# Kernel optimization log

Measured on AMD Instinct MI355X. Metric: run time of the kernel, lower is better.

## Reference

```python
import jax, jax.numpy as jnp
import numpy as np

B, T, D, H = 2, 2048, 1024, 4
DK, DV = 1024, 2048          # key_dim = d_model*expand_k, value_dim = d_model*expand_v
HK, HV = DK // H, DV // H    # 256, 512 per-head dims
LR = 16                      # gate_low_rank_dim
EPS = 1e-5
GATE_NORM = 16.0             # gate_logit_normalizer


def _xavier(k, shape, gain):
    fan_in, fan_out = shape
    lim = gain * np.sqrt(6.0 / (fan_in + fan_out))
    return jax.random.uniform(k, shape, jnp.float32, -lim, lim)


def setup_inputs() -> dict:
    key = jax.random.key(0)
    ks = jax.random.split(key, 10)
    g_qkv = 2 ** (-2.5)
    return {
        "x": jax.random.normal(ks[0], (B, T, D), jnp.float32),
        "Wq": _xavier(ks[1], (D, DK), g_qkv),
        "Wk": _xavier(ks[2], (D, DK), g_qkv),
        "Wv": _xavier(ks[3], (D, DV), g_qkv),
        "Wg": _xavier(ks[4], (D, DV), g_qkv),
        "gk_w1": _xavier(ks[5], (D, LR), g_qkv),
        "gk_w2": _xavier(ks[6], (LR, DK), g_qkv),
        "gk_b": jnp.zeros((DK,), jnp.float32),
        "Wo": _xavier(ks[7], (DV, D), 2 ** (-1)),
        "rms_w": jnp.ones((HV,), jnp.float32),
    }


def _gla_scan(q, k, v, g):
    # q,k,g: [T, hk]; v: [T, hv]. Recurrence S_t = diag(exp(g_t)) S_{t-1} + k_t v_t^T; o_t = q_t @ S_t
    S0 = jnp.zeros((q.shape[-1], v.shape[-1]), q.dtype)

    def step(S, inp):
        qt, kt, vt, gt = inp
        S = jnp.exp(gt)[:, None] * S + kt[:, None] * vt[None, :]
        return S, qt @ S

    return jax.lax.scan(step, S0, (q, k, v, g))[1]  # [T, hv]


def _forward(x, Wq, Wk, Wv, Wg, gk_w1, gk_w2, gk_b, Wo, rms_w):
    b, t = x.shape[0], x.shape[1]
    scale = HK ** -0.5
    # projections -> [b, h, t, d_head]
    q = (x @ Wq).reshape(b, t, H, HK).transpose(0, 2, 1, 3) * scale
    k = (x @ Wk).reshape(b, t, H, HK).transpose(0, 2, 1, 3)
    v = (x @ Wv).reshape(b, t, H, HV).transpose(0, 2, 1, 3)
    # low-rank forget gate, log-space, fp32
    gl = (x @ gk_w1) @ gk_w2 + gk_b
    g = (jax.nn.log_sigmoid(gl.astype(jnp.float32)) / GATE_NORM)
    g = g.reshape(b, t, H, HK).transpose(0, 2, 1, 3)
    # per-(batch, head) linear-attention recurrence
    o = jax.vmap(jax.vmap(_gla_scan))(q, k, v, g)  # [b, h, t, hv]
    # group RMSNorm over head_v_dim
    o = o.transpose(0, 2, 1, 3)  # [b, t, h, hv]
    o = o * jax.lax.rsqrt(jnp.mean(o * o, axis=-1, keepdims=True) + EPS) * rms_w
    # output gate (swish) + out projection
    o = o.reshape(b, t, DV) * jax.nn.silu(x @ Wg)
    return o @ Wo  # [b, t, d_model]


def reference(x, Wq, Wk, Wv, Wg, gk_w1, gk_w2, gk_b, Wo, rms_w):
    return _forward(x, Wq, Wk, Wv, Wg, gk_w1, gk_w2, gk_b, Wo, rms_w)
```

## Files before the change

kernel.cpp:

```cpp
#include <hip/hip_runtime.h>
#include <cstdint>
#include <cstddef>


typedef unsigned short u16;
typedef __attribute__((ext_vector_type(8))) short s8v;
typedef __attribute__((ext_vector_type(4))) short s4v;
typedef __attribute__((ext_vector_type(4))) float f4v;

__device__ __forceinline__ u16 f2b(float f) {
  unsigned u = __builtin_bit_cast(unsigned, f);
  unsigned r = u + 0x7FFFu + ((u >> 16) & 1u);
  return (u16)(r >> 16);
}
__device__ __forceinline__ float b2f(u16 h) {
  unsigned u = ((unsigned)h) << 16;
  return __builtin_bit_cast(float, u);
}

__device__ __forceinline__ void cp16(const void* g, void* l) {
  __builtin_amdgcn_global_load_lds(
      (const __attribute__((address_space(1))) unsigned int*)g,
      (__attribute__((address_space(3))) unsigned int*)l, 16, 0, 0);
}

__device__ __forceinline__ void stage_tile(const u16* g, int ld, u16* lds,
                                           int wv, int ln) {
  const int q = (ln & 3) ^ ((ln >> 3) & 3);
#pragma unroll
  for (int i = 0; i < 2; ++i) {
    const int c = wv * 2 + i;
    const u16* src = g + (size_t)(c * 16 + (ln >> 2)) * ld + q * 8;
    cp16(src, lds + c * 512);
  }
}

__device__ __forceinline__ void gemm_core(
    const u16* __restrict__ A, int lda, const u16* __restrict__ BT, int ldb,
    int K, u16* As, u16* Bs, f4v acc[4][4])
{
  const int tid = threadIdx.x;
  const int ln = tid & 63, wv = tid >> 6;
  const int arow = (wv >> 1) * 64 + (ln & 15);
  const int brow = (wv & 1) * 64 + (ln & 15);
  const int koff = (((ln >> 4) ^ ((ln >> 1) & 3)) * 8);
  const int nt = K >> 5;
  stage_tile(A, lda, As, wv, ln);
  stage_tile(BT, ldb, Bs, wv, ln);
  stage_tile(A + 32, lda, As + 4096, wv, ln);
  stage_tile(BT + 32, ldb, Bs + 4096, wv, ln);
  int slot = 0;
  for (int t = 0; t < nt; ++t) {
    if (t + 1 < nt) asm volatile("s_waitcnt vmcnt(4)" ::: "memory");
    else            asm volatile("s_waitcnt vmcnt(0)" ::: "memory");
    __builtin_amdgcn_s_barrier();
    __builtin_amdgcn_sched_barrier(0);
    const u16* Ab = As + slot * 4096;
    const u16* Bb = Bs + slot * 4096;
    s8v af[4], bf[4];
#pragma unroll
    for (int f = 0; f < 4; ++f)
      af[f] = *(const s8v*)(Ab + (arow + f * 16) * 32 + koff);
#pragma unroll
    for (int f = 0; f < 4; ++f)
      bf[f] = *(const s8v*)(Bb + (brow + f * 16) * 32 + koff);
#pragma unroll
    for (int mf = 0; mf < 4; ++mf)
#pragma unroll
      for (int nf = 0; nf < 4; ++nf)
        acc[mf][nf] = __builtin_amdgcn_mfma_f32_16x16x32_bf16(
            af[mf], bf[nf], acc[mf][nf], 0, 0, 0);
    __builtin_amdgcn_sched_barrier(0);
    __builtin_amdgcn_s_barrier();
    if (t + 2 < nt) {
      stage_tile(A + (t + 2) * 32, lda, As + slot * 4096, wv, ln);
      stage_tile(BT + (t + 2) * 32, ldb, Bs + slot * 4096, wv, ln);
    }
    slot ^= 1;
  }
}

__device__ __forceinline__ void frag_to_lds(u16* S, const f4v acc[4][4],
                                            int ln, int wv) {
  u16* q = S + wv * 4608;
#pragma unroll
  for (int mf = 0; mf < 4; ++mf)
#pragma unroll
    for (int nf = 0; nf < 4; ++nf)
#pragma unroll
      for (int r = 0; r < 4; ++r)
        q[(mf * 16 + ((ln >> 4) << 2) + r) * 72 + nf * 16 + (ln & 15)] =
            f2b(acc[mf][nf][r]);
}

__device__ __forceinline__ void frag_to_lds_T(u16* S, const f4v acc[4][4],
                                              int ln, int wv) {
  const int wr = wv >> 1, wc = wv & 1;
  u16* q = S + ((wc << 1) + wr) * 4608;
#pragma unroll
  for (int mf = 0; mf < 4; ++mf)
#pragma unroll
    for (int nf = 0; nf < 4; ++nf) {
      const int cl = nf * 16 + (ln & 15);
      const int rl = mf * 16 + ((ln >> 4) << 2);
      s4v o4;
#pragma unroll
      for (int r = 0; r < 4; ++r) o4[r] = (short)f2b(acc[mf][nf][r]);
      *(s4v*)(q + cl * 72 + rl) = o4;
    }
}

template <typename F>
__device__ __forceinline__ void epi_loop(u16* S, const f4v acc[4][4], F f) {
  const int tid = threadIdx.x;
  frag_to_lds(S, acc, tid & 63, tid >> 6);
  __syncthreads();
#pragma unroll
  for (int p = 0; p < 8; ++p) {
    const int r = p * 16 + (tid >> 4);
    const int c0 = (tid & 15) * 8;
    const int quad = ((r >> 6) << 1) + (c0 >> 6);
    s8v vv = *(const s8v*)(S + quad * 4608 + (r & 63) * 72 + (c0 & 63));
    f(r, c0, vv);
  }
}

template <typename F>
__device__ __forceinline__ void epi_loop_T(u16* S, const f4v acc[4][4], F f) {
  const int tid = threadIdx.x;
  frag_to_lds_T(S, acc, tid & 63, tid >> 6);
  __syncthreads();
#pragma unroll
  for (int p = 0; p < 8; ++p) {
    const int r = p * 16 + (tid >> 4);
    const int c0 = (tid & 15) * 8;
    const int quad = ((r >> 6) << 1) + (c0 >> 6);
    s8v vv = *(const s8v*)(S + quad * 4608 + (r & 63) * 72 + (c0 & 63));
    f(r, c0, vv);
  }
}

__global__ __launch_bounds__(256) void castw_all(
    const float* __restrict__ x, const float* __restrict__ Wq,
    const float* __restrict__ Wk, const float* __restrict__ Wv,
    const float* __restrict__ Wg, const float* __restrict__ Wo,
    u16* __restrict__ xb, u16* __restrict__ WTa, u16* __restrict__ WoT)
{
  __shared__ float t[32][33];
  const int id = blockIdx.x;
  if (id < 4096) {
    const int i = id * 256 + threadIdx.x;
    const float4 v = ((const float4*)x)[i];
    u16* p = xb + i * 4;
    p[0] = f2b(v.x); p[1] = f2b(v.y); p[2] = f2b(v.z); p[3] = f2b(v.w);
    return;
  }
  const int wid = id - 4096;
  const float* src; u16* dst; int R, C, local;
  if (wid < 1024)      { src = Wq; dst = WTa;           R = 1024; C = 1024; local = wid; }
  else if (wid < 2048) { src = Wk; dst = WTa + 1048576; R = 1024; C = 1024; local = wid - 1024; }
  else if (wid < 4096) { src = Wv; dst = WTa + 2097152; R = 1024; C = 2048; local = wid - 2048; }
  else if (wid < 6144) { src = Wg; dst = WTa + 4194304; R = 1024; C = 2048; local = wid - 4096; }
  else                 { src = Wo; dst = WoT;           R = 2048; C = 1024; local = wid - 6144; }
  const int nx = C >> 5;
  const int c0 = (local % nx) * 32, r0 = (local / nx) * 32;
  const int lx = threadIdx.x & 31, ly = threadIdx.x >> 5;
#pragma unroll
  for (int i = 0; i < 32; i += 8)
    t[ly + i][lx] = src[(size_t)(r0 + ly + i) * C + c0 + lx];
  __syncthreads();
#pragma unroll
  for (int i = 0; i < 32; i += 8)
    dst[(size_t)(c0 + ly + i) * R + r0 + lx] = f2b(t[lx][ly + i]);
}

__global__ __launch_bounds__(256) void trans_kt(
    const u16* __restrict__ kt, u16* __restrict__ ktT)
{
  __shared__ u16 t[32][33];
  const int id = blockIdx.x;
  const int z = id >> 9, local = id & 511;
  const int c0 = (local & 7) * 32, r0 = (local >> 3) * 32;
  const size_t boff = (size_t)z * 2048 * 256;
  const int lx = threadIdx.x & 31, ly = threadIdx.x >> 5;
#pragma unroll
  for (int i = 0; i < 32; i += 8)
    t[ly + i][lx] = kt[boff + (size_t)(r0 + ly + i) * 256 + c0 + lx];
  __syncthreads();
#pragma unroll
  for (int i = 0; i < 32; i += 8)
    ktT[boff + (size_t)(c0 + ly + i) * 2048 + r0 + lx] = t[lx][ly + i];
}

__global__ __launch_bounds__(256) void lowrank1(
    const float* __restrict__ x, const float* __restrict__ w1,
    float* __restrict__ tmp)
{
  const int idx = blockIdx.x * 256 + threadIdx.x;
  const int m = idx >> 4, i = idx & 15;
  const float* xr = x + (size_t)m * 1024;
  float acc = 0.f;
#pragma unroll 4
  for (int kk = 0; kk < 1024; kk += 4) {
    const float4 xv = *(const float4*)(xr + kk);
    acc = fmaf(xv.x, w1[(kk + 0) * 16 + i], acc);
    acc = fmaf(xv.y, w1[(kk + 1) * 16 + i], acc);
    acc = fmaf(xv.z, w1[(kk + 2) * 16 + i], acc);
    acc = fmaf(xv.w, w1[(kk + 3) * 16 + i], acc);
  }
  tmp[idx] = acc;
}

__global__ __launch_bounds__(256) void gate_cum(
    const float* __restrict__ tmp, const float* __restrict__ w2,
    const float* __restrict__ bias, u16* __restrict__ dq, u16* __restrict__ dk,
    float* __restrict__ Dc)
{
  __shared__ float ls_t[2048];
  const int b = blockIdx.y >> 4, c = blockIdx.y & 15;
  const int h = blockIdx.x;
  const int i = threadIdx.x;
  const int n = h * 256 + i;
  const int bh = b * 4 + h;
  const float* tp = tmp + ((size_t)(b * 2048 + c * 128)) * 16;
#pragma unroll
  for (int r = 0; r < 8; ++r) ls_t[r * 256 + threadIdx.x] = tp[r * 256 + threadIdx.x];
  __syncthreads();
  float w2c[16];
#pragma unroll
  for (int r = 0; r < 16; ++r) w2c[r] = w2[r * 1024 + n];
  const float bn = bias[n];
  const size_t base = ((size_t)bh * 2048 + c * 128) * 256 + i;
  float B = 0.f;
  for (int t = 0; t < 128; ++t) {
    float gl = bn;
    const float* tr = ls_t + t * 16;
#pragma unroll
    for (int r = 0; r < 16; ++r) gl = fmaf(tr[r], w2c[r], gl);
    const float ls = fminf(gl, 0.f) - log1pf(expf(-fabsf(gl)));
    B += ls * 0.0625f;
    const float eB = expf(B);
    dq[base + (size_t)t * 256] = f2b(eB);
    dk[base + (size_t)t * 256] = f2b(1.f / eB);
  }
  Dc[(bh * 16 + c) * 256 + i] = expf(B);
}

__global__ __launch_bounds__(256) void proj_all(
    const u16* __restrict__ xb, const u16* __restrict__ WT,
    const u16* __restrict__ dq, const u16* __restrict__ dk,
    u16* __restrict__ qt, u16* __restrict__ kt,
    u16* __restrict__ vT, u16* __restrict__ gpre)
{
  __shared__ __align__(16) u16 S[18432];
  u16* As = S; u16* Bs = S + 8192;
  const int id = blockIdx.x;
  const int xcd = id & 7, jb = id >> 3;
  const int m0 = (jb / 6) * 128;
  const int n0 = (xcd * 6 + (jb % 6)) * 128;
  f4v acc[4][4];
#pragma unroll
  for (int zi = 0; zi < 4; ++zi)
#pragma unroll
    for (int zj = 0; zj < 4; ++zj) acc[zi][zj] = (f4v){0.f, 0.f, 0.f, 0.f};
  gemm_core(xb + (size_t)m0 * 1024, 1024, WT + (size_t)n0 * 1024, 1024, 1024,
            As, Bs, acc);
  const int bb = m0 >> 11;
  const int t0 = m0 & 2047;
  if (n0 < 1024) {
    epi_loop(S, acc, [&](int r, int c0, s8v vv) {
      const int t = t0 + r;
      const int n = n0 + c0;
      const int bh = bb * 4 + (n >> 8);
      const size_t off = ((size_t)bh * 2048 + t) * 256 + (n & 255);
      const s8v dv = *(const s8v*)(dq + off);
      s8v o8;
#pragma unroll
      for (int e = 0; e < 8; ++e)
        o8[e] = (short)f2b(b2f((u16)vv[e]) * 0.0625f * b2f((u16)dv[e]));
      *(s8v*)(qt + off) = o8;
    });
  } else if (n0 < 2048) {
    epi_loop(S, acc, [&](int r, int c0, s8v vv) {
      const int t = t0 + r;
      const int nn = n0 + c0 - 1024;
      const int bh = bb * 4 + (nn >> 8);
      const size_t off = ((size_t)bh * 2048 + t) * 256 + (nn & 255);
      const s8v dv = *(const s8v*)(dk + off);
      s8v o8;
#pragma unroll
      for (int e = 0; e < 8; ++e)
        o8[e] = (short)f2b(b2f((u16)vv[e]) * b2f((u16)dv[e]));
      *(s8v*)(kt + off) = o8;
    });
  } else if (n0 < 4096) {
    const int nn0 = n0 - 2048;
    const int bh = bb * 4 + (nn0 >> 9);
    const int jj0 = nn0 & 511;
    epi_loop_T(S, acc, [&](int r, int c0, s8v vv) {
      *(s8v*)(vT + ((size_t)(bh * 512 + jj0 + r)) * 2048 + t0 + c0) = vv;
    });
  } else {
    epi_loop(S, acc, [&](int r, int c0, s8v vv) {
      *(s8v*)(gpre + (size_t)(m0 + r) * 2048 + (n0 + c0 - 4096)) = vv;
    });
  }
}

__global__ __launch_bounds__(256) void scan_gemms(
    const u16* __restrict__ vT, const u16* __restrict__ ktT,
    const u16* __restrict__ qt, const u16* __restrict__ kt,
    u16* __restrict__ UT, u16* __restrict__ Aw)
{
  __shared__ __align__(16) u16 S[18432];
  u16* As = S; u16* Bs = S + 8192;
  const int bhc = blockIdx.y, bh = bhc >> 4, c = bhc & 15;
  f4v acc[4][4];
#pragma unroll
  for (int zi = 0; zi < 4; ++zi)
#pragma unroll
    for (int zj = 0; zj < 4; ++zj) acc[zi][zj] = (f4v){0.f, 0.f, 0.f, 0.f};
  if (blockIdx.x < 8) {
    const int mt = blockIdx.x >> 1, nt = blockIdx.x & 1;
    gemm_core(vT + ((size_t)bh * 512 + mt * 128) * 2048 + c * 128, 2048,
              ktT + ((size_t)bh * 256 + nt * 128) * 2048 + c * 128, 2048, 128,
              As, Bs, acc);
    epi_loop(S, acc, [&](int r, int c0, s8v vv) {
      const int j = mt * 128 + r;
      const int i = nt * 128 + c0;
      *(s8v*)(UT + (((size_t)(bh * 512 + j)) * 16 + c) * 256 + i) = vv;
    });
  } else {
    const size_t base = ((size_t)bh * 2048 + c * 128) * 256;
    gemm_core(qt + base, 256, kt + base, 256, 256, As, Bs, acc);
    u16* Ap = Aw + (size_t)bhc * 16384;
    epi_loop(S, acc, [&](int r, int c0, s8v vv) {
      s8v o8;
#pragma unroll
      for (int e = 0; e < 8; ++e)
        o8[e] = (c0 + e <= r) ? vv[e] : (short)0;
      *(s8v*)(Ap + r * 128 + c0) = o8;
    });
  }
}

__global__ __launch_bounds__(256) void state_scan(
    u16* __restrict__ UT, const float* __restrict__ Dc)
{
  const int blk = blockIdx.x;
  const int bh = blk >> 9, j = blk & 511;
  const int i = threadIdx.x;
  u16* Up = UT + ((size_t)(bh * 512 + j)) * 16 * 256 + i;
  const float* Dp = Dc + bh * 16 * 256 + i;
  float Sa = 0.f;
  for (int c = 0; c < 16; ++c) {
    const float u = b2f(Up[c * 256]);
    Up[c * 256] = f2b(Sa);
    Sa = Dp[c * 256] * (Sa + u);
  }
}

__global__ __launch_bounds__(256) void intra_k(
    const u16* __restrict__ Aw, const u16* __restrict__ qt,
    const u16* __restrict__ vT, const u16* __restrict__ UT, u16* __restrict__ ob)
{
  __shared__ __align__(16) u16 S[18432];
  u16* As = S; u16* Bs = S + 8192;
  const int jt = blockIdx.x;
  const int bhc = blockIdx.y, bh = bhc >> 4, c = bhc & 15;
  f4v acc[4][4];
#pragma unroll
  for (int zi = 0; zi < 4; ++zi)
#pragma unroll
    for (int zj = 0; zj < 4; ++zj) acc[zi][zj] = (f4v){0.f, 0.f, 0.f, 0.f};
  gemm_core(Aw + (size_t)bhc * 16384, 128,
            vT + ((size_t)bh * 512 + jt * 128) * 2048 + c * 128, 2048, 128,
            As, Bs, acc);
  gemm_core(qt + ((size_t)bh * 2048 + c * 128) * 256, 256,
            UT + ((size_t)(bh * 512 + jt * 128)) * 4096 + (size_t)c * 256, 4096, 256,
            As, Bs, acc);
  const int b = bh >> 2, h = bh & 3;
  epi_loop(S, acc, [&](int r, int c0, s8v vv) {
    const int t = c * 128 + r;
    const int j = jt * 128 + c0;
    *(s8v*)(ob + ((size_t)(b * 2048 + t)) * 2048 + h * 512 + j) = vv;
  });
}

__global__ __launch_bounds__(256) void rms_silu(
    u16* __restrict__ o, const u16* __restrict__ gpre, const float* __restrict__ w)
{
  const int grp = blockIdx.x * 4 + (threadIdx.x >> 6);
  const int lane = threadIdx.x & 63;
  const size_t base = (size_t)(grp >> 2) * 2048 + (grp & 3) * 512;
  float xv[8];
  float ss = 0.f;
#pragma unroll
  for (int i = 0; i < 8; ++i) {
    xv[i] = b2f(o[base + i * 64 + lane]);
    ss = fmaf(xv[i], xv[i], ss);
  }
#pragma unroll
  for (int off = 1; off < 64; off <<= 1) ss += __shfl_xor(ss, off, 64);
  const float r = rsqrtf(ss * (1.f / 512.f) + 1e-5f);
#pragma unroll
  for (int i = 0; i < 8; ++i) {
    const int cidx = i * 64 + lane;
    const float gp = b2f(gpre[base + cidx]);
    const float sig = 1.f / (1.f + expf(-gp));
    o[base + cidx] = f2b(xv[i] * r * w[cidx] * gp * sig);
  }
}

__global__ __launch_bounds__(256) void gemm_out(
    const u16* __restrict__ ob, const u16* __restrict__ WoT,
    float* __restrict__ pout)
{
  __shared__ __align__(16) u16 S[18432];
  u16* As = S; u16* Bs = S + 8192;
  const int id = blockIdx.x;
  const int wg = (id & 7) * 64 + (id >> 3);
  const int ks = wg >> 8;
  const int tt = wg & 255;
  const int m0 = (tt & 31) * 128, n0 = (tt >> 5) * 128;
  f4v acc[4][4];
#pragma unroll
  for (int zi = 0; zi < 4; ++zi)
#pragma unroll
    for (int zj = 0; zj < 4; ++zj) acc[zi][zj] = (f4v){0.f, 0.f, 0.f, 0.f};
  gemm_core(ob + (size_t)m0 * 2048 + ks * 1024, 2048,
            WoT + (size_t)n0 * 2048 + ks * 1024, 2048, 1024, As, Bs, acc);
  const int tid = threadIdx.x;
  const int ln = tid & 63, wv = tid >> 6;
  const int wr = wv >> 1, wc = wv & 1;
  float* po = pout + (size_t)ks * 4194304;
#pragma unroll
  for (int mf = 0; mf < 4; ++mf)
#pragma unroll
    for (int nf = 0; nf < 4; ++nf)
#pragma unroll
      for (int r = 0; r < 4; ++r) {
        const int m = m0 + wr * 64 + mf * 16 + ((ln >> 4) << 2) + r;
        const int n = n0 + wc * 64 + nf * 16 + (ln & 15);
        po[(size_t)m * 1024 + n] = acc[mf][nf][r];
      }
}

__global__ __launch_bounds__(256) void reduce_out(
    const float* __restrict__ p, float* __restrict__ out)
{
  const int i = blockIdx.x * 256 + threadIdx.x;
  const float4 a = ((const float4*)p)[i];
  const float4 b = ((const float4*)(p + 4194304))[i];
  ((float4*)out)[i] = make_float4(a.x + b.x, a.y + b.y, a.z + b.z, a.w + b.w);
}

extern "C" void kernel_launch(void* const* d_in, const int* in_sizes, int n_in,
                              void* d_out, int out_size, void* d_ws, size_t ws_size,
                              hipStream_t stream) {
  const float* x    = (const float*)d_in[0];
  const float* Wq   = (const float*)d_in[1];
  const float* Wk   = (const float*)d_in[2];
  const float* Wv   = (const float*)d_in[3];
  const float* Wg   = (const float*)d_in[4];
  const float* w1   = (const float*)d_in[5];
  const float* w2   = (const float*)d_in[6];
  const float* gb   = (const float*)d_in[7];
  const float* Wo   = (const float*)d_in[8];
  const float* rmsw = (const float*)d_in[9];
  float* out = (float*)d_out;

  char* W = (char*)d_ws;
  u16*   xb   = (u16*)W;   W += (size_t)8  << 20;
  u16*   WTa  = (u16*)W;   W += (size_t)12 << 20;
  u16*   WoT  = (u16*)W;   W += (size_t)4  << 20;
  u16*   qt   = (u16*)W;   W += (size_t)8  << 20;
  u16*   kt   = (u16*)W;   W += (size_t)8  << 20;
  u16*   vT   = (u16*)W;   W += (size_t)16 << 20;
  u16*   ktT  = (u16*)W;   W += (size_t)8  << 20;
  u16*   gpre = (u16*)W;   W += (size_t)16 << 20;
  float* tmp  = (float*)W; W += (size_t)256 << 10;
  float* Dc   = (float*)W; W += (size_t)128 << 10;
  u16*   dq   = (u16*)W;   W += (size_t)8  << 20;
  u16*   dk   = (u16*)W;   W += (size_t)8  << 20;
  u16*   UT   = (u16*)W;   W += (size_t)32 << 20;
  u16*   Aw   = (u16*)W;   W += (size_t)4  << 20;
  u16*   ob   = (u16*)W;   W += (size_t)16 << 20;
  float* pout = (float*)W; W += (size_t)32 << 20;

  hipLaunchKernelGGL(lowrank1, dim3(256), dim3(256), 0, stream, x, w1, tmp);
  hipLaunchKernelGGL(gate_cum, dim3(4, 32), dim3(256), 0, stream,
                     tmp, w2, gb, dq, dk, Dc);

  hipLaunchKernelGGL(castw_all, dim3(12288), dim3(256), 0, stream,
                     x, Wq, Wk, Wv, Wg, Wo, xb, WTa, WoT);

  hipLaunchKernelGGL(proj_all, dim3(1536), dim3(256), 0, stream,
                     xb, WTa, dq, dk, qt, kt, vT, gpre);

  hipLaunchKernelGGL(trans_kt, dim3(4096), dim3(256), 0, stream, kt, ktT);

  hipLaunchKernelGGL(scan_gemms, dim3(9, 128), dim3(256), 0, stream,
                     vT, ktT, qt, kt, UT, Aw);
  hipLaunchKernelGGL(state_scan, dim3(4096), dim3(256), 0, stream, UT, Dc);
  hipLaunchKernelGGL(intra_k, dim3(4, 128), dim3(256), 0, stream, Aw, qt, vT, UT, ob);

  hipLaunchKernelGGL(rms_silu, dim3(4096), dim3(256), 0, stream, ob, gpre, rmsw);
  hipLaunchKernelGGL(gemm_out, dim3(512), dim3(256), 0, stream, ob, WoT, pout);
  hipLaunchKernelGGL(reduce_out, dim3(4096), dim3(256), 0, stream, pout, out);
}
```

Before: 259.0 us.

## Widen projection GEMM tile to 128x256 with double-buffered swizzled LDS pipeline

Replaces the 128x128-tile projection GEMM with a 128x256 tile kernel, so each wave computes a 4x8 MFMA fragment block. It halves the grid, stages K slices of 32 with async global-to-LDS copies into two buffers using an XOR swizzle, and writes the epilogue back in four 64-column passes through shared memory. The aim is higher arithmetic intensity and less redundant A-tile loading, at the cost of more accumulator registers (launch bounds set to 2 blocks per CU) and fewer blocks in flight.

Result: no change. 263.2 us (+1.6%).

```diff
diff --git a/kernel.cpp b/kernel.cpp
--- a/kernel.cpp
+++ b/kernel.cpp
@@ -93,23 +93,6 @@
             f2b(acc[mf][nf][r]);
 }
 
-__device__ __forceinline__ void frag_to_lds_T(u16* S, const f4v acc[4][4],
-                                              int ln, int wv) {
-  const int wr = wv >> 1, wc = wv & 1;
-  u16* q = S + ((wc << 1) + wr) * 4608;
-#pragma unroll
-  for (int mf = 0; mf < 4; ++mf)
-#pragma unroll
-    for (int nf = 0; nf < 4; ++nf) {
-      const int cl = nf * 16 + (ln & 15);
-      const int rl = mf * 16 + ((ln >> 4) << 2);
-      s4v o4;
-#pragma unroll
-      for (int r = 0; r < 4; ++r) o4[r] = (short)f2b(acc[mf][nf][r]);
-      *(s4v*)(q + cl * 72 + rl) = o4;
-    }
-}
-
 template <typename F>
 __device__ __forceinline__ void epi_loop(u16* S, const f4v acc[4][4], F f) {
   const int tid = threadIdx.x;
@@ -125,18 +108,160 @@
   }
 }
 
-template <typename F>
-__device__ __forceinline__ void epi_loop_T(u16* S, const f4v acc[4][4], F f) {
+__device__ __forceinline__ void stage_wide(const u16* A, const u16* BT,
+                                           u16* slot, int wv, int ln) {
+  const int q = (ln & 3) ^ ((ln >> 3) & 3);
+#pragma unroll
+  for (int i = 0; i < 2; ++i) {
+    const int c = wv * 2 + i;
+    cp16(A + (size_t)(c * 16 + (ln >> 2)) * 1024 + q * 8, slot + c * 512);
+  }
+#pragma unroll
+  for (int i = 0; i < 4; ++i) {
+    const int c = wv * 4 + i;
+    cp16(BT + (size_t)(c * 16 + (ln >> 2)) * 1024 + q * 8,
+         slot + 4096 + c * 512);
+  }
+}
+
+__global__ __launch_bounds__(256, 2) void proj_wide(
+    const u16* __restrict__ xb, const u16* __restrict__ WT,
+    const u16* __restrict__ dq, const u16* __restrict__ dk,
+    u16* __restrict__ qt, u16* __restrict__ kt,
+    u16* __restrict__ vT, u16* __restrict__ gpre)
+{
+  __shared__ __align__(16) u16 S[24576];
   const int tid = threadIdx.x;
-  frag_to_lds_T(S, acc, tid & 63, tid >> 6);
-  __syncthreads();
-#pragma unroll
-  for (int p = 0; p < 8; ++p) {
-    const int r = p * 16 + (tid >> 4);
-    const int c0 = (tid & 15) * 8;
-    const int quad = ((r >> 6) << 1) + (c0 >> 6);
-    s8v vv = *(const s8v*)(S + quad * 4608 + (r & 63) * 72 + (c0 & 63));
-    f(r, c0, vv);
+  const int ln = tid & 63, wv = tid >> 6;
+  const int wr = wv >> 1, wc = wv & 1;
+  const int id = blockIdx.x;
+  const int xcd = id & 7, jb = id >> 3;
+  const int m0 = (jb / 3) * 128;
+  const int n0 = (xcd * 3 + (jb % 3)) * 256;
+  const u16* A = xb + (size_t)m0 * 1024;
+  const u16* BT = WT + (size_t)n0 * 1024;
+  f4v acc[4][8];
+#pragma unroll
+  for (int zi = 0; zi < 4; ++zi)
+#pragma unroll
+    for (int zj = 0; zj < 8; ++zj) acc[zi][zj] = (f4v){0.f, 0.f, 0.f, 0.f};
+  const int arow = wr * 64 + (ln & 15);
+  const int brow = wc * 128 + (ln & 15);
+  const int koff = (((ln >> 4) ^ ((ln >> 1) & 3)) * 8);
+  stage_wide(A, BT, S, wv, ln);
+  stage_wide(A + 32, BT + 32, S + 12288, wv, ln);
+  int slot = 0;
+  for (int t = 0; t < 32; ++t) {
+    if (t < 31) asm volatile("s_waitcnt vmcnt(6)" ::: "memory");
+    else        asm volatile("s_waitcnt vmcnt(0)" ::: "memory");
+    __builtin_amdgcn_s_barrier();
+    __builtin_amdgcn_sched_barrier(0);
+    const u16* Ab = S + slot * 12288;
+    const u16* Bb = Ab + 4096;
+    s8v af[4], bf[8];
+#pragma unroll
+    for (int f = 0; f < 4; ++f)
+      af[f] = *(const s8v*)(Ab + (arow + f * 16) * 32 + koff);
+#pragma unroll
+    for (int f = 0; f < 8; ++f)
+      bf[f] = *(const s8v*)(Bb + (brow + f * 16) * 32 + koff);
+#pragma unroll
+    for (int mf = 0; mf < 4; ++mf)
+#pragma unroll
+      for (int nf = 0; nf < 8; ++nf)
+        acc[mf][nf] = __builtin_amdgcn_mfma_f32_16x16x32_bf16(
+            af[mf], bf[nf], acc[mf][nf], 0, 0, 0);
+    __builtin_amdgcn_sched_barrier(0);
+    __builtin_amdgcn_s_barrier();
+    if (t + 2 < 32)
+      stage_wide(A + (t + 2) * 32, BT + (t + 2) * 32, S + slot * 12288, wv, ln);
+    slot ^= 1;
+  }
+  const int bb = m0 >> 11, t0 = m0 & 2047;
+  const bool isv = (n0 >= 2048) && (n0 < 4096);
+#pragma unroll
+  for (int p = 0; p < 4; ++p) {
+    __syncthreads();
+    if (wc == (p >> 1)) {
+      const int nfb = (p & 1) * 4;
+      if (!isv) {
+#pragma unroll
+        for (int mf = 0; mf < 4; ++mf)
+#pragma unroll
+          for (int nf4 = 0; nf4 < 4; ++nf4)
+#pragma unroll
+            for (int rr = 0; rr < 4; ++rr)
+              S[(wr * 64 + mf * 16 + ((ln >> 4) << 2) + rr) * 72 +
+                nf4 * 16 + (ln & 15)] = f2b(acc[mf][nfb + nf4][rr]);
+      } else {
+#pragma unroll
+        for (int mf = 0; mf < 4; ++mf)
+#pragma unroll
+          for (int nf4 = 0; nf4 < 4; ++nf4) {
+            const int cl = nf4 * 16 + (ln & 15);
+            const int rl = wr * 64 + mf * 16 + ((ln >> 4) << 2);
+            s4v o4;
+#pragma unroll
+            for (int rr = 0; rr < 4; ++rr)
+              o4[rr] = (short)f2b(acc[mf][nfb + nf4][rr]);
+            *(s4v*)(S + cl * 136 + rl) = o4;
+          }
+      }
+    }
+    __syncthreads();
+    const int ncol = n0 + p * 64;
+    if (n0 < 1024) {
+      const int bh = bb * 4 + (n0 >> 8);
+#pragma unroll
+      for (int ps = 0; ps < 4; ++ps) {
+        const int r = ps * 32 + (tid >> 3);
+        const int c0q = (tid & 7) * 8;
+        s8v vv = *(const s8v*)(S + r * 72 + c0q);
+        const size_t off =
+            ((size_t)bh * 2048 + t0 + r) * 256 + (ncol & 255) + c0q;
+        const s8v dv = *(const s8v*)(dq + off);
+        s8v o8;
+#pragma unroll
+        for (int e = 0; e < 8; ++e)
+          o8[e] = (short)f2b(b2f((u16)vv[e]) * 0.0625f * b2f((u16)dv[e]));
+        *(s8v*)(qt + off) = o8;
+      }
+    } else if (n0 < 2048) {
+      const int bh = bb * 4 + ((n0 - 1024) >> 8);
+#pragma unroll
+      for (int ps = 0; ps < 4; ++ps) {
+        const int r = ps * 32 + (tid >> 3);
+        const int c0q = (tid & 7) * 8;
+        s8v vv = *(const s8v*)(S + r * 72 + c0q);
+        const size_t off =
+            ((size_t)bh * 2048 + t0 + r) * 256 + ((ncol - 1024) & 255) + c0q;
+        const s8v dv = *(const s8v*)(dk + off);
+        s8v o8;
+#pragma unroll
+        for (int e = 0; e < 8; ++e)
+          o8[e] = (short)f2b(b2f((u16)vv[e]) * b2f((u16)dv[e]));
+        *(s8v*)(kt + off) = o8;
+      }
+    } else if (n0 < 4096) {
+      const int nn = ncol - 2048;
+      const int bh = bb * 4 + (nn >> 9);
+      const int jj0 = nn & 511;
+#pragma unroll
+      for (int ps = 0; ps < 4; ++ps) {
+        const int jq = ps * 16 + (tid >> 4);
+        const int tq = (tid & 15) * 8;
+        s8v vv = *(const s8v*)(S + jq * 136 + tq);
+        *(s8v*)(vT + ((size_t)(bh * 512 + jj0 + jq)) * 2048 + t0 + tq) = vv;
+      }
+    } else {
+#pragma unroll
+      for (int ps = 0; ps < 4; ++ps) {
+        const int r = ps * 32 + (tid >> 3);
+        const int c0q = (tid & 7) * 8;
+        s8v vv = *(const s8v*)(S + r * 72 + c0q);
+        *(s8v*)(gpre + (size_t)(m0 + r) * 2048 + (ncol - 4096) + c0q) = vv;
+      }
+    }
   }
 }
 
@@ -244,67 +369,6 @@
     dk[base + (size_t)t * 256] = f2b(1.f / eB);
   }
   Dc[(bh * 16 + c) * 256 + i] = expf(B);
-}
-
-__global__ __launch_bounds__(256) void proj_all(
-    const u16* __restrict__ xb, const u16* __restrict__ WT,
-    const u16* __restrict__ dq, const u16* __restrict__ dk,
-    u16* __restrict__ qt, u16* __restrict__ kt,
-    u16* __restrict__ vT, u16* __restrict__ gpre)
-{
-  __shared__ __align__(16) u16 S[18432];
-  u16* As = S; u16* Bs = S + 8192;
-  const int id = blockIdx.x;
-  const int xcd = id & 7, jb = id >> 3;
-  const int m0 = (jb / 6) * 128;
-  const int n0 = (xcd * 6 + (jb % 6)) * 128;
-  f4v acc[4][4];
-#pragma unroll
-  for (int zi = 0; zi < 4; ++zi)
-#pragma unroll
-    for (int zj = 0; zj < 4; ++zj) acc[zi][zj] = (f4v){0.f, 0.f, 0.f, 0.f};
-  gemm_core(xb + (size_t)m0 * 1024, 1024, WT + (size_t)n0 * 1024, 1024, 1024,
-            As, Bs, acc);
-  const int bb = m0 >> 11;
-  const int t0 = m0 & 2047;
-  if (n0 < 1024) {
-    epi_loop(S, acc, [&](int r, int c0, s8v vv) {
-      const int t = t0 + r;
-      const int n = n0 + c0;
-      const int bh = bb * 4 + (n >> 8);
-      const size_t off = ((size_t)bh * 2048 + t) * 256 + (n & 255);
-      const s8v dv = *(const s8v*)(dq + off);
-      s8v o8;
-#pragma unroll
-      for (int e = 0; e < 8; ++e)
-        o8[e] = (short)f2b(b2f((u16)vv[e]) * 0.0625f * b2f((u16)dv[e]));
-      *(s8v*)(qt + off) = o8;
-    });
-  } else if (n0 < 2048) {
-    epi_loop(S, acc, [&](int r, int c0, s8v vv) {
-      const int t = t0 + r;
-      const int nn = n0 + c0 - 1024;
-      const int bh = bb * 4 + (nn >> 8);
-      const size_t off = ((size_t)bh * 2048 + t) * 256 + (nn & 255);
-      const s8v dv = *(const s8v*)(dk + off);
-      s8v o8;
-#pragma unroll
-      for (int e = 0; e < 8; ++e)
-        o8[e] = (short)f2b(b2f((u16)vv[e]) * b2f((u16)dv[e]));
-      *(s8v*)(kt + off) = o8;
-    });
-  } else if (n0 < 4096) {
-    const int nn0 = n0 - 2048;
-    const int bh = bb * 4 + (nn0 >> 9);
-    const int jj0 = nn0 & 511;
-    epi_loop_T(S, acc, [&](int r, int c0, s8v vv) {
-      *(s8v*)(vT + ((size_t)(bh * 512 + jj0 + r)) * 2048 + t0 + c0) = vv;
-    });
-  } else {
-    epi_loop(S, acc, [&](int r, int c0, s8v vv) {
-      *(s8v*)(gpre + (size_t)(m0 + r) * 2048 + (n0 + c0 - 4096)) = vv;
-    });
-  }
 }
 
 __global__ __launch_bounds__(256) void scan_gemms(
@@ -495,7 +559,7 @@
   hipLaunchKernelGGL(castw_all, dim3(12288), dim3(256), 0, stream,
                      x, Wq, Wk, Wv, Wg, Wo, xb, WTa, WoT);
 
-  hipLaunchKernelGGL(proj_all, dim3(1536), dim3(256), 0, stream,
+  hipLaunchKernelGGL(proj_wide, dim3(768), dim3(256), 0, stream,
                      xb, WTa, dq, dk, qt, kt, vT, gpre);
 
   hipLaunchKernelGGL(trans_kt, dim3(4096), dim3(256), 0, stream, kt, ktT);
```

## Fuse low-rank gate projection into cast kernel and k transpose into projection epilogue

Applied to the files above, without the earlier changes.

The low-rank x@gk_w1 computation moves into extra blocks of the weight/activation cast kernel, which removes a separate launch. The standalone k-transpose kernel is also removed: the k-projection epilogue now transposes its gated tile through LDS and writes ktT directly, saving a full read and write of k. The cost is extra LDS round trips and barriers in the k epilogue, plus scalar scattered LDS stores that may bank-conflict.

Result: slower. 324.5 us (+25.3%).

```diff
diff --git a/kernel.cpp b/kernel.cpp
--- a/kernel.cpp
+++ b/kernel.cpp
@@ -144,7 +144,9 @@
     const float* __restrict__ x, const float* __restrict__ Wq,
     const float* __restrict__ Wk, const float* __restrict__ Wv,
     const float* __restrict__ Wg, const float* __restrict__ Wo,
-    u16* __restrict__ xb, u16* __restrict__ WTa, u16* __restrict__ WoT)
+    const float* __restrict__ w1,
+    u16* __restrict__ xb, u16* __restrict__ WTa, u16* __restrict__ WoT,
+    float* __restrict__ tmp)
 {
   __shared__ float t[32][33];
   const int id = blockIdx.x;
@@ -153,6 +155,22 @@
     const float4 v = ((const float4*)x)[i];
     u16* p = xb + i * 4;
     p[0] = f2b(v.x); p[1] = f2b(v.y); p[2] = f2b(v.z); p[3] = f2b(v.w);
+    return;
+  }
+  if (id >= 12288) {
+    const int idx = (id - 12288) * 256 + threadIdx.x;
+    const int m = idx >> 4, i = idx & 15;
+    const float* xr = x + (size_t)m * 1024;
+    float acc = 0.f;
+#pragma unroll 4
+    for (int kk = 0; kk < 1024; kk += 4) {
+      const float4 xv = *(const float4*)(xr + kk);
+      acc = fmaf(xv.x, w1[(kk + 0) * 16 + i], acc);
+      acc = fmaf(xv.y, w1[(kk + 1) * 16 + i], acc);
+      acc = fmaf(xv.z, w1[(kk + 2) * 16 + i], acc);
+      acc = fmaf(xv.w, w1[(kk + 3) * 16 + i], acc);
+    }
+    tmp[idx] = acc;
     return;
   }
   const int wid = id - 4096;
@@ -174,43 +192,6 @@
     dst[(size_t)(c0 + ly + i) * R + r0 + lx] = f2b(t[lx][ly + i]);
 }
 
-__global__ __launch_bounds__(256) void trans_kt(
-    const u16* __restrict__ kt, u16* __restrict__ ktT)
-{
-  __shared__ u16 t[32][33];
-  const int id = blockIdx.x;
-  const int z = id >> 9, local = id & 511;
-  const int c0 = (local & 7) * 32, r0 = (local >> 3) * 32;
-  const size_t boff = (size_t)z * 2048 * 256;
-  const int lx = threadIdx.x & 31, ly = threadIdx.x >> 5;
-#pragma unroll
-  for (int i = 0; i < 32; i += 8)
-    t[ly + i][lx] = kt[boff + (size_t)(r0 + ly + i) * 256 + c0 + lx];
-  __syncthreads();
-#pragma unroll
-  for (int i = 0; i < 32; i += 8)
-    ktT[boff + (size_t)(c0 + ly + i) * 2048 + r0 + lx] = t[lx][ly + i];
-}
-
-__global__ __launch_bounds__(256) void lowrank1(
-    const float* __restrict__ x, const float* __restrict__ w1,
-    float* __restrict__ tmp)
-{
-  const int idx = blockIdx.x * 256 + threadIdx.x;
-  const int m = idx >> 4, i = idx & 15;
-  const float* xr = x + (size_t)m * 1024;
-  float acc = 0.f;
-#pragma unroll 4
-  for (int kk = 0; kk < 1024; kk += 4) {
-    const float4 xv = *(const float4*)(xr + kk);
-    acc = fmaf(xv.x, w1[(kk + 0) * 16 + i], acc);
-    acc = fmaf(xv.y, w1[(kk + 1) * 16 + i], acc);
-    acc = fmaf(xv.z, w1[(kk + 2) * 16 + i], acc);
-    acc = fmaf(xv.w, w1[(kk + 3) * 16 + i], acc);
-  }
-  tmp[idx] = acc;
-}
-
 __global__ __launch_bounds__(256) void gate_cum(
     const float* __restrict__ tmp, const float* __restrict__ w2,
     const float* __restrict__ bias, u16* __restrict__ dq, u16* __restrict__ dk,
@@ -249,7 +230,7 @@
 __global__ __launch_bounds__(256) void proj_all(
     const u16* __restrict__ xb, const u16* __restrict__ WT,
     const u16* __restrict__ dq, const u16* __restrict__ dk,
-    u16* __restrict__ qt, u16* __restrict__ kt,
+    u16* __restrict__ qt, u16* __restrict__ kt, u16* __restrict__ ktT,
     u16* __restrict__ vT, u16* __restrict__ gpre)
 {
   __shared__ __align__(16) u16 S[18432];
@@ -269,10 +250,9 @@
   const int t0 = m0 & 2047;
   if (n0 < 1024) {
     epi_loop(S, acc, [&](int r, int c0, s8v vv) {
-      const int t = t0 + r;
       const int n = n0 + c0;
       const int bh = bb * 4 + (n >> 8);
-      const size_t off = ((size_t)bh * 2048 + t) * 256 + (n & 255);
+      const size_t off = ((size_t)bh * 2048 + t0 + r) * 256 + (n & 255);
       const s8v dv = *(const s8v*)(dq + off);
       s8v o8;
 #pragma unroll
@@ -281,18 +261,49 @@
       *(s8v*)(qt + off) = o8;
     });
   } else if (n0 < 2048) {
-    epi_loop(S, acc, [&](int r, int c0, s8v vv) {
-      const int t = t0 + r;
-      const int nn = n0 + c0 - 1024;
-      const int bh = bb * 4 + (nn >> 8);
-      const size_t off = ((size_t)bh * 2048 + t) * 256 + (nn & 255);
+    const int nn0 = n0 - 1024;
+    const int bh = bb * 4 + (nn0 >> 8);
+    const int i0 = nn0 & 255;
+    const int tid = threadIdx.x;
+    s8v keep[8];
+    frag_to_lds(S, acc, tid & 63, tid >> 6);
+    __syncthreads();
+#pragma unroll
+    for (int p = 0; p < 8; ++p) {
+      const int r = p * 16 + (tid >> 4);
+      const int c0 = (tid & 15) * 8;
+      const int quad = ((r >> 6) << 1) + (c0 >> 6);
+      s8v vv = *(const s8v*)(S + quad * 4608 + (r & 63) * 72 + (c0 & 63));
+      const size_t off = ((size_t)bh * 2048 + t0 + r) * 256 + i0 + c0;
       const s8v dv = *(const s8v*)(dk + off);
       s8v o8;
 #pragma unroll
       for (int e = 0; e < 8; ++e)
         o8[e] = (short)f2b(b2f((u16)vv[e]) * b2f((u16)dv[e]));
       *(s8v*)(kt + off) = o8;
-    });
+      keep[p] = o8;
+    }
+    __syncthreads();
+#pragma unroll
+    for (int p = 0; p < 8; ++p) {
+      const int r = p * 16 + (tid >> 4);
+      const int c0 = (tid & 15) * 8;
+#pragma unroll
+      for (int e = 0; e < 8; ++e) {
+        const int c = c0 + e;
+        S[(((c >> 6) << 1) + (r >> 6)) * 4608 + (c & 63) * 72 + (r & 63)] =
+            (u16)keep[p][e];
+      }
+    }
+    __syncthreads();
+#pragma unroll
+    for (int p = 0; p < 8; ++p) {
+      const int i = p * 16 + (tid >> 4);
+      const int tt = (tid & 15) * 8;
+      const int quad = ((i >> 6) << 1) + (tt >> 6);
+      s8v vv = *(const s8v*)(S + quad * 4608 + (i & 63) * 72 + (tt & 63));
+      *(s8v*)(ktT + ((size_t)(bh * 256 + i0 + i)) * 2048 + t0 + tt) = vv;
+    }
   } else if (n0 < 4096) {
     const int nn0 = n0 - 2048;
     const int bh = bb * 4 + (nn0 >> 9);
@@ -488,17 +499,13 @@
   u16*   ob   = (u16*)W;   W += (size_t)16 << 20;
   float* pout = (float*)W; W += (size_t)32 << 20;
 
-  hipLaunchKernelGGL(lowrank1, dim3(256), dim3(256), 0, stream, x, w1, tmp);
+  hipLaunchKernelGGL(castw_all, dim3(12544), dim3(256), 0, stream,
+                     x, Wq, Wk, Wv, Wg, Wo, w1, xb, WTa, WoT, tmp);
   hipLaunchKernelGGL(gate_cum, dim3(4, 32), dim3(256), 0, stream,
                      tmp, w2, gb, dq, dk, Dc);
 
-  hipLaunchKernelGGL(castw_all, dim3(12288), dim3(256), 0, stream,
-                     x, Wq, Wk, Wv, Wg, Wo, xb, WTa, WoT);
-
   hipLaunchKernelGGL(proj_all, dim3(1536), dim3(256), 0, stream,
-                     xb, WTa, dq, dk, qt, kt, vT, gpre);
-
-  hipLaunchKernelGGL(trans_kt, dim3(4096), dim3(256), 0, stream, kt, ktT);
+                     xb, WTa, dq, dk, qt, kt, ktT, vT, gpre);
 
   hipLaunchKernelGGL(scan_gemms, dim3(9, 128), dim3(256), 0, stream,
                      vT, ktT, qt, kt, UT, Aw);
```
